# Kernel tuning notes

Measured on AMD Instinct MI355X. Metric: run time of the kernel, lower is better.

The kernel has to match this reference:

```python
import jax, jax.numpy as jnp
import numpy as np


def setup_inputs() -> dict:
    key = jax.random.key(0)
    k1, k2 = jax.random.split(key)
    B, S, N, D = 4, 8, 2048, 3
    pred_points = jax.random.normal(k1, (B, S, N, D), dtype=jnp.float32)
    target_points = jax.random.normal(k2, (B, S, N, D), dtype=jnp.float32)
    return {"pred_points": pred_points, "target_points": target_points}


def reference(pred_points, target_points):
    # pred_points, target_points: [B, S, N, 3]
    seq_len = pred_points.shape[1]
    # Pairwise Euclidean distances via the GEMM identity |p-t|^2 = |p|^2 + |t|^2 - 2 p.t
    p2 = jnp.sum(pred_points * pred_points, axis=-1)      # [B,S,N]
    t2 = jnp.sum(target_points * target_points, axis=-1)  # [B,S,M]
    cross = jnp.einsum('bsnd,bsmd->bsnm', pred_points, target_points)  # [B,S,N,M]
    d2 = p2[..., :, None] + t2[..., None, :] - 2.0 * cross
    d = jnp.sqrt(jnp.maximum(d2, 0.0))  # [B,S,N,M]
    # Bidirectional nearest-neighbor min + mean over points
    min_p2t = jnp.min(d, axis=3)  # [B,S,N]
    min_t2p = jnp.min(d, axis=2)  # [B,S,M]
    chamfer = jnp.mean(min_p2t, axis=2) + jnp.mean(min_t2p, axis=2)  # [B,S]
    total_loss = jnp.sum(chamfer, axis=1)  # [B] (sum over timesteps)
    # reduction == 'mean'
    return jnp.mean(total_loss) / seq_len
```

## Files before the change

kernel.cpp:

```cpp
#include <hip/hip_runtime.h>
#include <math.h>

#define N_PTS   2048
#define BLOCK   128
#define NQ      16
#define SLAB    128
#define NSLAB   (N_PTS / SLAB)

typedef float v2f __attribute__((ext_vector_type(2)));

__global__ __launch_bounds__(BLOCK) void chamfer_min_kernel(
    const float* __restrict__ pred,
    const float* __restrict__ tgt,
    float* __restrict__ ws)
{
    __shared__ v2f shx[SLAB / 2], shy[SLAB / 2], shz[SLAB / 2], shw[SLAB / 2];

    const int bs   = blockIdx.x;
    const int dir  = blockIdx.y;
    const int slab = blockIdx.z;
    const int tid  = threadIdx.x;

    const float* Abase = (dir ? tgt : pred) + (size_t)bs * N_PTS * 3;
    const float* Bbase = (dir ? pred : tgt) + (size_t)bs * N_PTS * 3;

    {
        const int j = slab * SLAB + tid;
        const float x = Bbase[3 * j + 0];
        const float y = Bbase[3 * j + 1];
        const float z = Bbase[3 * j + 2];
        ((float*)shx)[tid] = x;
        ((float*)shy)[tid] = y;
        ((float*)shz)[tid] = z;
        ((float*)shw)[tid] = x * x + y * y + z * z;
    }
    __syncthreads();

    v2f nx2[NQ], ny2[NQ], nz2[NQ];
    float p2[NQ], best[NQ];
    #pragma unroll
    for (int k = 0; k < NQ; ++k) {
        const int q = tid + BLOCK * k;
        const float px = Abase[3 * q + 0];
        const float py = Abase[3 * q + 1];
        const float pz = Abase[3 * q + 2];
        const float ax = -2.0f * px, ay = -2.0f * py, az = -2.0f * pz;
        nx2[k] = (v2f){ax, ax};
        ny2[k] = (v2f){ay, ay};
        nz2[k] = (v2f){az, az};
        p2[k] = px * px + py * py + pz * pz;
        best[k] = 3.4e38f;
    }

    #pragma unroll 2
    for (int jj = 0; jj < SLAB / 2; ++jj) {
        const v2f tx = shx[jj];
        const v2f ty = shy[jj];
        const v2f tz = shz[jj];
        const v2f tw = shw[jj];
        #pragma unroll
        for (int k = 0; k < NQ; ++k) {
            const v2f v = __builtin_elementwise_fma(nx2[k], tx,
                          __builtin_elementwise_fma(ny2[k], ty,
                          __builtin_elementwise_fma(nz2[k], tz, tw)));
            best[k] = fminf(best[k], fminf(v.x, v.y));
        }
    }

    float* dst = ws + ((size_t)(dir * NSLAB + slab) * 32 + bs) * N_PTS;
    #pragma unroll
    for (int k = 0; k < NQ; ++k)
        dst[tid + BLOCK * k] = p2[k] + best[k];
}

__global__ __launch_bounds__(256) void chamfer_finalize_kernel(
    const float* __restrict__ ws,
    float* __restrict__ out)
{
    __shared__ float red[4];
    const int i = blockIdx.x * 256 + threadIdx.x;
    const int dir = i >> 16;
    const int bsq = i & 0xFFFF;

    float m = 3.4e38f;
    #pragma unroll
    for (int s = 0; s < NSLAB; ++s)
        m = fminf(m, ws[(size_t)(dir * NSLAB + s) * 65536 + bsq]);
    float d = sqrtf(fmaxf(m, 0.0f));

    for (int off = 32; off > 0; off >>= 1)
        d += __shfl_down(d, off, 64);
    const int tid = threadIdx.x;
    if ((tid & 63) == 0) red[tid >> 6] = d;
    __syncthreads();
    if (tid == 0) {
        const float blk = red[0] + red[1] + red[2] + red[3];
        atomicAdd(out, blk * (1.0f / 65536.0f));
    }
}

extern "C" void kernel_launch(void* const* d_in, const int* in_sizes, int n_in,
                              void* d_out, int out_size, void* d_ws, size_t ws_size,
                              hipStream_t stream) {
    const float* pred = (const float*)d_in[0];
    const float* tgt  = (const float*)d_in[1];
    float* out = (float*)d_out;
    float* ws = (float*)d_ws;

    hipMemsetAsync(out, 0, sizeof(float), stream);

    dim3 grid(32, 2, NSLAB);
    chamfer_min_kernel<<<grid, BLOCK, 0, stream>>>(pred, tgt, ws);

    chamfer_finalize_kernel<<<131072 / 256, 256, 0, stream>>>(ws, out);
}
```

Before: 88.08 us.

## Merge per-slab minima with global atomicMin and use wider blocks

The min kernel no longer writes one partial-minimum array per slab. Each block clamps its squared distances to non-negative and merges them into a single shared buffer with atomicMin on the float bit pattern, after a memset to 0xFF. The finalize kernel then reads one vectorised float4 per thread instead of scanning 16 slabs. Block size goes to 256 threads with 8 queries per thread and a launch-bounds occupancy hint. This adds contended atomics and an extra memset in exchange for much less workspace traffic.

```diff
diff --git a/kernel.cpp b/kernel.cpp
--- a/kernel.cpp
+++ b/kernel.cpp
@@ -2,17 +2,17 @@
 #include <math.h>
 
 #define N_PTS   2048
-#define BLOCK   128
-#define NQ      16
+#define BLOCK   256
+#define NQ      8
 #define SLAB    128
 #define NSLAB   (N_PTS / SLAB)
 
 typedef float v2f __attribute__((ext_vector_type(2)));
 
-__global__ __launch_bounds__(BLOCK) void chamfer_min_kernel(
+__global__ __launch_bounds__(BLOCK, 4) void chamfer_min_kernel(
     const float* __restrict__ pred,
     const float* __restrict__ tgt,
-    float* __restrict__ ws)
+    unsigned int* __restrict__ wsmin)
 {
     __shared__ v2f shx[SLAB / 2], shy[SLAB / 2], shz[SLAB / 2], shw[SLAB / 2];
 
@@ -24,7 +24,7 @@
     const float* Abase = (dir ? tgt : pred) + (size_t)bs * N_PTS * 3;
     const float* Bbase = (dir ? pred : tgt) + (size_t)bs * N_PTS * 3;
 
-    {
+    if (tid < SLAB) {
         const int j = slab * SLAB + tid;
         const float x = Bbase[3 * j + 0];
         const float y = Bbase[3 * j + 1];
@@ -67,31 +67,27 @@
         }
     }
 
-    float* dst = ws + ((size_t)(dir * NSLAB + slab) * 32 + bs) * N_PTS;
+    const int base = (dir * 32 + bs) * N_PTS;
     #pragma unroll
-    for (int k = 0; k < NQ; ++k)
-        dst[tid + BLOCK * k] = p2[k] + best[k];
+    for (int k = 0; k < NQ; ++k) {
+        const float d2 = fmaxf(p2[k] + best[k], 0.0f);
+        atomicMin(&wsmin[base + tid + BLOCK * k], __float_as_uint(d2));
+    }
 }
 
 __global__ __launch_bounds__(256) void chamfer_finalize_kernel(
-    const float* __restrict__ ws,
+    const float4* __restrict__ wsmin,
     float* __restrict__ out)
 {
     __shared__ float red[4];
     const int i = blockIdx.x * 256 + threadIdx.x;
-    const int dir = i >> 16;
-    const int bsq = i & 0xFFFF;
-
-    float m = 3.4e38f;
-    #pragma unroll
-    for (int s = 0; s < NSLAB; ++s)
-        m = fminf(m, ws[(size_t)(dir * NSLAB + s) * 65536 + bsq]);
-    float d = sqrtf(fmaxf(m, 0.0f));
+    const float4 t = wsmin[i];
+    float s = sqrtf(t.x) + sqrtf(t.y) + sqrtf(t.z) + sqrtf(t.w);
 
     for (int off = 32; off > 0; off >>= 1)
-        d += __shfl_down(d, off, 64);
+        s += __shfl_down(s, off, 64);
     const int tid = threadIdx.x;
-    if ((tid & 63) == 0) red[tid >> 6] = d;
+    if ((tid & 63) == 0) red[tid >> 6] = s;
     __syncthreads();
     if (tid == 0) {
         const float blk = red[0] + red[1] + red[2] + red[3];
@@ -105,12 +101,14 @@
     const float* pred = (const float*)d_in[0];
     const float* tgt  = (const float*)d_in[1];
     float* out = (float*)d_out;
-    float* ws = (float*)d_ws;
+    unsigned int* wsmin = (unsigned int*)d_ws;
 
+    hipMemsetAsync(wsmin, 0xFF, (size_t)131072 * sizeof(unsigned int), stream);
     hipMemsetAsync(out, 0, sizeof(float), stream);
 
     dim3 grid(32, 2, NSLAB);
-    chamfer_min_kernel<<<grid, BLOCK, 0, stream>>>(pred, tgt, ws);
+    chamfer_min_kernel<<<grid, BLOCK, 0, stream>>>(pred, tgt, wsmin);
 
-    chamfer_finalize_kernel<<<131072 / 256, 256, 0, stream>>>(ws, out);
+    chamfer_finalize_kernel<<<131072 / (256 * 4), 256, 0, stream>>>(
+        (const float4*)wsmin, out);
 }
```

Result: faster. 84.03 us (-4.6%).
